# Optimization experiments

Measured on AMD Instinct MI355X. Metric: run time of the kernel, lower is better.

Reference implementation:

```python
import jax, jax.numpy as jnp
import numpy as np

EPS = 1e-12
LAMDA = 1.0
MAX_ITER = 10


def setup_inputs() -> dict:
    key = jax.random.key(0)
    k1, k2 = jax.random.split(key)
    B, L1, L2, D = 64, 1024, 1024, 256
    x1 = jax.random.normal(k1, (B, L1, D), dtype=jnp.float32)
    x2 = jax.random.normal(k2, (B, L2, D), dtype=jnp.float32)
    return {"x1": x1, "x2": x2}


def _cos(x1, x2):
    # batched cosine similarity: [B, L1, L2]
    M = jnp.einsum('bik,bjk->bij', x1, x2)
    a = jnp.sqrt(jnp.sum(x1 * x1, axis=-1, keepdims=True))  # [B, L1, 1]
    b = jnp.sqrt(jnp.sum(x2 * x2, axis=-1, keepdims=True))  # [B, L2, 1]
    norm = a * jnp.swapaxes(b, 1, 2)                          # [B, L1, L2]
    return M / (norm + EPS)


def reference(x1, x2):
    B, L1, _ = x1.shape
    L2 = x2.shape[1]
    M = 1.0 - _cos(x1, x2)          # [B, L1, L2] cost matrix
    K = jnp.exp(-M * LAMDA)
    w1 = jnp.full((B, L1, 1), 1.0 / L1, dtype=x1.dtype)
    w2 = jnp.full((B, L2, 1), 1.0 / L2, dtype=x1.dtype)
    ui = jnp.ones((B, L1, 1), dtype=x1.dtype)
    vi = jnp.ones((B, L2, 1), dtype=x1.dtype)
    Kt = jnp.swapaxes(K, 1, 2)      # [B, L2, L1]

    def body(_, carry):
        ui, vi = carry
        vi = w2 / (jnp.matmul(Kt, ui) + EPS)
        ui = w1 / (jnp.matmul(K, vi) + EPS)
        return (ui, vi)

    ui, vi = jax.lax.fori_loop(0, MAX_ITER, body, (ui, vi))
    G = ui * K * jnp.swapaxes(vi, 1, 2)   # transport plan [B, L1, L2]
    G_max = jnp.max(G, axis=(-1, -2), keepdims=True)
    G_min = jnp.min(G, axis=(-1, -2), keepdims=True)
    G = (G - G_min) / (G_max - G_min + EPS)
    return G * M
```

## Files before the change

kernel.cpp:

```cpp
#include <hip/hip_runtime.h>
#include <hip/hip_bf16.h>
#include <hip/hip_fp8.h>


#define EPSV 1e-12f
#define W1 0.0009765625f

typedef short  short8 __attribute__((ext_vector_type(8)));
typedef float  f32x4  __attribute__((ext_vector_type(4)));
typedef float  f32x2v __attribute__((ext_vector_type(2)));

__device__ __forceinline__ float rcpf_(float x) {
#if __has_builtin(__builtin_amdgcn_rcpf)
  return __builtin_amdgcn_rcpf(x);
#else
  return 1.0f / x;
#endif
}
__device__ __forceinline__ float rsqf_(float x) {
#if __has_builtin(__builtin_amdgcn_rsqf)
  return __builtin_amdgcn_rsqf(x);
#else
  return rsqrtf(x);
#endif
}

__device__ __forceinline__ unsigned char enc1(float x) {
#if __has_builtin(__builtin_amdgcn_cvt_pk_fp8_f32)
  int v = __builtin_amdgcn_cvt_pk_fp8_f32(x, x, 0, false);
  return (unsigned char)(v & 0xff);
#else
  __hip_fp8_e4m3 q(x); return (unsigned char)q.__x;
#endif
}
__device__ __forceinline__ float dec1(unsigned char b) {
#if __has_builtin(__builtin_amdgcn_cvt_f32_fp8)
  return __builtin_amdgcn_cvt_f32_fp8((int)b, 0);
#else
  __hip_fp8_e4m3 q; q.__x = (__hip_fp8_storage_t)b; return (float)q;
#endif
}
__device__ __forceinline__ unsigned pack4fp8(float a, float b, float c, float d) {
#if __has_builtin(__builtin_amdgcn_cvt_pk_fp8_f32)
  int v = __builtin_amdgcn_cvt_pk_fp8_f32(a, b, 0, false);
  v = __builtin_amdgcn_cvt_pk_fp8_f32(c, d, v, true);
  return (unsigned)v;
#else
  return (unsigned)enc1(a) | ((unsigned)enc1(b) << 8) |
         ((unsigned)enc1(c) << 16) | ((unsigned)enc1(d) << 24);
#endif
}
__device__ __forceinline__ void unpack4fp8(unsigned v, float* f) {
#if __has_builtin(__builtin_amdgcn_cvt_pk_f32_fp8)
  f32x2v p;
  p = __builtin_amdgcn_cvt_pk_f32_fp8((int)v, false); f[0] = p[0]; f[1] = p[1];
  p = __builtin_amdgcn_cvt_pk_f32_fp8((int)v, true);  f[2] = p[0]; f[3] = p[1];
#else
  #pragma unroll
  for (int i = 0; i < 4; ++i) f[i] = dec1((unsigned char)((v >> (i * 8)) & 0xff));
#endif
}
__device__ __forceinline__ void decode16(uint4 d, float* f) {
  unpack4fp8(d.x, f); unpack4fp8(d.y, f + 4);
  unpack4fp8(d.z, f + 8); unpack4fp8(d.w, f + 12);
}
__device__ __forceinline__ float dot16u(uint4 d, const float* s) {
#if __has_builtin(__builtin_amdgcn_cvt_pk_f32_fp8)
  f32x2v p; float a = 0.f;
  p = __builtin_amdgcn_cvt_pk_f32_fp8((int)d.x, false); a += p[0]*s[0]  + p[1]*s[1];
  p = __builtin_amdgcn_cvt_pk_f32_fp8((int)d.x, true);  a += p[0]*s[2]  + p[1]*s[3];
  p = __builtin_amdgcn_cvt_pk_f32_fp8((int)d.y, false); a += p[0]*s[4]  + p[1]*s[5];
  p = __builtin_amdgcn_cvt_pk_f32_fp8((int)d.y, true);  a += p[0]*s[6]  + p[1]*s[7];
  p = __builtin_amdgcn_cvt_pk_f32_fp8((int)d.z, false); a += p[0]*s[8]  + p[1]*s[9];
  p = __builtin_amdgcn_cvt_pk_f32_fp8((int)d.z, true);  a += p[0]*s[10] + p[1]*s[11];
  p = __builtin_amdgcn_cvt_pk_f32_fp8((int)d.w, false); a += p[0]*s[12] + p[1]*s[13];
  p = __builtin_amdgcn_cvt_pk_f32_fp8((int)d.w, true);  a += p[0]*s[14] + p[1]*s[15];
  return a;
#else
  float f[16]; decode16(d, f);
  float a = 0.f;
  #pragma unroll
  for (int k = 0; k < 16; ++k) a += f[k] * s[k];
  return a;
#endif
}
__device__ __forceinline__ void axpy16u(uint4 d, float u, float* pacc) {
#if __has_builtin(__builtin_amdgcn_cvt_pk_f32_fp8)
  f32x2v p;
  p = __builtin_amdgcn_cvt_pk_f32_fp8((int)d.x, false); pacc[0]  += p[0]*u; pacc[1]  += p[1]*u;
  p = __builtin_amdgcn_cvt_pk_f32_fp8((int)d.x, true);  pacc[2]  += p[0]*u; pacc[3]  += p[1]*u;
  p = __builtin_amdgcn_cvt_pk_f32_fp8((int)d.y, false); pacc[4]  += p[0]*u; pacc[5]  += p[1]*u;
  p = __builtin_amdgcn_cvt_pk_f32_fp8((int)d.y, true);  pacc[6]  += p[0]*u; pacc[7]  += p[1]*u;
  p = __builtin_amdgcn_cvt_pk_f32_fp8((int)d.z, false); pacc[8]  += p[0]*u; pacc[9]  += p[1]*u;
  p = __builtin_amdgcn_cvt_pk_f32_fp8((int)d.z, true);  pacc[10] += p[0]*u; pacc[11] += p[1]*u;
  p = __builtin_amdgcn_cvt_pk_f32_fp8((int)d.w, false); pacc[12] += p[0]*u; pacc[13] += p[1]*u;
  p = __builtin_amdgcn_cvt_pk_f32_fp8((int)d.w, true);  pacc[14] += p[0]*u; pacc[15] += p[1]*u;
#else
  float f[16]; decode16(d, f);
  #pragma unroll
  for (int k = 0; k < 16; ++k) pacc[k] += f[k] * u;
#endif
}

__device__ __forceinline__ short8 ld_cvt8_sq(const float* p, float* sq) {
  float4 f0 = *(const float4*)p;
  float4 f1 = *(const float4*)(p + 4);
  *sq += f0.x * f0.x + f0.y * f0.y + f0.z * f0.z + f0.w * f0.w
       + f1.x * f1.x + f1.y * f1.y + f1.z * f1.z + f1.w * f1.w;
  float2 p0; p0.x = f0.x; p0.y = f0.y;
  float2 p1; p1.x = f0.z; p1.y = f0.w;
  float2 p2; p2.x = f1.x; p2.y = f1.y;
  float2 p3; p3.x = f1.z; p3.y = f1.w;
  __hip_bfloat162 h0 = __float22bfloat162_rn(p0);
  __hip_bfloat162 h1 = __float22bfloat162_rn(p1);
  __hip_bfloat162 h2_ = __float22bfloat162_rn(p2);
  __hip_bfloat162 h3 = __float22bfloat162_rn(p3);
  short2 a = *(short2*)&h0, b = *(short2*)&h1, c = *(short2*)&h2_, d = *(short2*)&h3;
  short8 r;
  r[0] = a.x; r[1] = a.y; r[2] = b.x; r[3] = b.y;
  r[4] = c.x; r[5] = c.y; r[6] = d.x; r[7] = d.y;
  return r;
}

__global__ __launch_bounds__(256) void diag_kernel(float* __restrict__ out,
                                                   float val, int n) {
  int stride = gridDim.x * 256;
  for (int i = blockIdx.x * 256 + threadIdx.x; i < n; i += stride) out[i] = val;
}

__global__ __launch_bounds__(256) void gemm_kernel(
    const float* __restrict__ x1, const float* __restrict__ x2,
    unsigned char* __restrict__ K8g, unsigned char* __restrict__ R8g,
    unsigned* __restrict__ mm, _Float16* __restrict__ p0) {
  __shared__ __align__(16) unsigned short smem[2 * 128 * 64];
  __shared__ float asq[128], bsq[128];
  __shared__ float csum[4][128];
  unsigned short* As = smem;
  unsigned short* Bs = smem + 128 * 64;
  int bid = blockIdx.x;
  int b = bid >> 6, tile = bid & 63;
  int ti = (tile >> 3) << 7, tj = (tile & 7) << 7;
  int t = threadIdx.x, lane = t & 63, wave = t >> 6;
  int wr = (wave >> 1) << 6, wc = (wave & 1) << 6;
  const float* Ag = x1 + ((size_t)(b * 1024 + ti)) * 256;
  const float* Bg = x2 + ((size_t)(b * 1024 + tj)) * 256;

  if (bid == 0 && t < 128) mm[t] = (t < 64) ? 0u : 0x7f800000u;

  f32x4 acc[4][4];
  f32x4 zero = {0.f, 0.f, 0.f, 0.f};
  #pragma unroll
  for (int m = 0; m < 4; ++m)
    #pragma unroll
    for (int n = 0; n < 4; ++n) acc[m][n] = zero;

  float sqa[4] = {0.f, 0.f, 0.f, 0.f};
  float sqb[4] = {0.f, 0.f, 0.f, 0.f};
  short8 ra[4], rb[4];
  #pragma unroll
  for (int c = 0; c < 4; ++c) {
    int ch = t + (c << 8); int row = ch >> 3, kg = ch & 7;
    ra[c] = ld_cvt8_sq(Ag + row * 256 + kg * 8, &sqa[c]);
    rb[c] = ld_cvt8_sq(Bg + row * 256 + kg * 8, &sqb[c]);
  }

  for (int k0 = 0; k0 < 4; ++k0) {
    __syncthreads();
    #pragma unroll
    for (int c = 0; c < 4; ++c) {
      int ch = t + (c << 8); int row = ch >> 3, kg = ch & 7;
      int kgs = kg ^ (row & 7);
      *(short8*)(As + row * 64 + kgs * 8) = ra[c];
      *(short8*)(Bs + row * 64 + kgs * 8) = rb[c];
    }
    __syncthreads();
    if (k0 < 3) {
      #pragma unroll
      for (int c = 0; c < 4; ++c) {
        int ch = t + (c << 8); int row = ch >> 3, kg = ch & 7;
        ra[c] = ld_cvt8_sq(Ag + row * 256 + (k0 + 1) * 64 + kg * 8, &sqa[c]);
        rb[c] = ld_cvt8_sq(Bg + row * 256 + (k0 + 1) * 64 + kg * 8, &sqb[c]);
      }
    }
    #pragma unroll
    for (int ks = 0; ks < 2; ++ks) {
      short8 af[4], bfr[4];
      #pragma unroll
      for (int m = 0; m < 4; ++m) {
        int row = wr + m * 16 + (lane & 15);
        int c16 = (ks << 2) + (lane >> 4);
        af[m] = *(const short8*)(As + row * 64 + ((c16 ^ (row & 7)) << 3));
      }
      #pragma unroll
      for (int n = 0; n < 4; ++n) {
        int row = wc + n * 16 + (lane & 15);
        int c16 = (ks << 2) + (lane >> 4);
        bfr[n] = *(const short8*)(Bs + row * 64 + ((c16 ^ (row & 7)) << 3));
      }
      #pragma unroll
      for (int m = 0; m < 4; ++m)
        #pragma unroll
        for (int n = 0; n < 4; ++n)
          acc[m][n] = __builtin_amdgcn_mfma_f32_16x16x32_bf16(bfr[n], af[m], acc[m][n], 0, 0, 0);
    }
  }
  __syncthreads();
  #pragma unroll
  for (int c = 0; c < 4; ++c) {
    float sa = sqa[c], sb = sqb[c];
    sa += __shfl_xor(sa, 1, 64); sb += __shfl_xor(sb, 1, 64);
    sa += __shfl_xor(sa, 2, 64); sb += __shfl_xor(sb, 2, 64);
    sa += __shfl_xor(sa, 4, 64); sb += __shfl_xor(sb, 4, 64);
    if ((t & 7) == 0) {
      int row = (t + (c << 8)) >> 3;
      asq[row] = sa; bsq[row] = sb;
    }
  }
  __syncthreads();

  float ira[4];
  #pragma unroll
  for (int m = 0; m < 4; ++m)
    ira[m] = rsqf_(asq[wr + m * 16 + (lane & 15)]);
  float irb[4][4];
  #pragma unroll
  for (int n = 0; n < 4; ++n)
    #pragma unroll
    for (int q = 0; q < 4; ++q)
      irb[n][q] = rsqf_(bsq[wc + n * 16 + ((lane >> 4) << 2) + q]);
  float csn[4][4];
  #pragma unroll
  for (int n = 0; n < 4; ++n)
    #pragma unroll
    for (int q = 0; q < 4; ++q) csn[n][q] = 0.f;
  size_t kbase = ((size_t)b << 20);
  #pragma unroll
  for (int m = 0; m < 4; ++m) {
    size_t rowoff = kbase + (size_t)(ti + wr + m * 16 + (lane & 15)) * 1024 + tj + wc + ((lane >> 4) << 2);
    #pragma unroll
    for (int n = 0; n < 4; ++n) {
      float kv[4];
      #pragma unroll
      for (int q = 0; q < 4; ++q) {
        float cosv = acc[m][n][q] * ira[m] * irb[n][q];
        kv[q] = __expf(cosv - 1.0f);
        csn[n][q] += kv[q];
      }
      unsigned pk = pack4fp8(kv[0], kv[1], kv[2], kv[3]);
      float kd[4];
      unpack4fp8(pk, kd);
      float rr[4];
      #pragma unroll
      for (int q = 0; q < 4; ++q) rr[q] = kv[q] * rcpf_(kd[q]) - 1.0f;
      unsigned pr = pack4fp8(rr[0], rr[1], rr[2], rr[3]);
      *(unsigned*)(K8g + rowoff + n * 16) = pk;
      *(unsigned*)(R8g + rowoff + n * 16) = pr;
    }
  }
  #pragma unroll
  for (int n = 0; n < 4; ++n)
    #pragma unroll
    for (int q = 0; q < 4; ++q) {
      float c_ = csn[n][q];
      c_ += __shfl_xor(c_, 1, 64);
      c_ += __shfl_xor(c_, 2, 64);
      c_ += __shfl_xor(c_, 4, 64);
      c_ += __shfl_xor(c_, 8, 64);
      if ((lane & 15) == 0)
        csum[wave][wc + n * 16 + ((lane >> 4) << 2) + q] = c_;
    }
  __syncthreads();
  if (t < 128) {
    float s_ = csum[t >> 6][t] + csum[2 + (t >> 6)][t];
    p0[((size_t)b << 13) + ((size_t)(ti >> 7) << 10) + tj + t] = (_Float16)s_;
  }
}

template<int BSHIFT, int NSRC>
__global__ __launch_bounds__(1024) void fused1024_kernel(
    const unsigned char* __restrict__ K8, const _Float16* __restrict__ src,
    _Float16* __restrict__ dst) {
  int bid = blockIdx.x;
  int b = bid >> 2, s = bid & 3;
  int t = threadIdx.x, lane = t & 63, w = t >> 6;
  __shared__ float sv[1024];
  __shared__ float plds[8][1024];
  {
    int col = t;
    const _Float16* sp = src + ((size_t)b << BSHIFT) + col;
    float y = 0.f;
    #pragma unroll
    for (int j = 0; j < NSRC; ++j) y += (float)sp[j << 10];
    sv[col] = W1 / (y + EPSV);
  }
  __syncthreads();
  float svr[16];
  {
    float4 s0 = *(const float4*)&sv[lane * 16];
    float4 s1 = *(const float4*)&sv[lane * 16 + 4];
    float4 s2 = *(const float4*)&sv[lane * 16 + 8];
    float4 s3 = *(const float4*)&sv[lane * 16 + 12];
    svr[0] = s0.x;  svr[1] = s0.y;  svr[2]  = s0.z;  svr[3]  = s0.w;
    svr[4] = s1.x;  svr[5] = s1.y;  svr[6]  = s1.z;  svr[7]  = s1.w;
    svr[8] = s2.x;  svr[9] = s2.y;  svr[10] = s2.z;  svr[11] = s2.w;
    svr[12] = s3.x; svr[13] = s3.y; svr[14] = s3.z;  svr[15] = s3.w;
  }
  float pacc[16];
  #pragma unroll
  for (int k = 0; k < 16; ++k) pacc[k] = 0.f;
  const unsigned char* kp = K8 + ((size_t)b << 20) + (size_t)(s * 256 + w) * 1024 + lane * 16;
  uint4 c0 = *(const uint4*)(kp);
  uint4 c1 = *(const uint4*)(kp + 16384);
  for (int p = 0; p < 8; ++p) {
    uint4 n0, n1_;
    if (p < 7) {
      n0 = *(const uint4*)(kp + (size_t)(2 * p + 2) * 16384);
      n1_ = *(const uint4*)(kp + (size_t)(2 * p + 3) * 16384);
    }
    float d0 = dot16u(c0, svr);
    float d1 = dot16u(c1, svr);
    #pragma unroll
    for (int off = 1; off < 64; off <<= 1) {
      d0 += __shfl_xor(d0, off, 64);
      d1 += __shfl_xor(d1, off, 64);
    }
    float u0 = W1 / (d0 + EPSV);
    float u1 = W1 / (d1 + EPSV);
    axpy16u(c0, u0, pacc);
    axpy16u(c1, u1, pacc);
    c0 = n0; c1 = n1_;
  }
  if (w < 8) {
    *(float4*)&plds[w][lane * 16]      = *(float4*)&pacc[0];
    *(float4*)&plds[w][lane * 16 + 4]  = *(float4*)&pacc[4];
    *(float4*)&plds[w][lane * 16 + 8]  = *(float4*)&pacc[8];
    *(float4*)&plds[w][lane * 16 + 12] = *(float4*)&pacc[12];
  }
  __syncthreads();
  if (w >= 8) {
    float* pl = &plds[w - 8][lane * 16];
    #pragma unroll
    for (int k = 0; k < 16; ++k) pl[k] += pacc[k];
  }
  __syncthreads();
  {
    int col = t;
    float sum = 0.f;
    #pragma unroll
    for (int i = 0; i < 8; ++i) sum += plds[i][col];
    dst[((size_t)b << 12) + (s << 10) + col] = (_Float16)sum;
  }
}

template<int FINAL>
__global__ __launch_bounds__(512) void fused512_kernel(
    const unsigned char* __restrict__ K8, const unsigned char* __restrict__ R8,
    const _Float16* __restrict__ src, _Float16* __restrict__ dst,
    float* __restrict__ zb, unsigned* __restrict__ mm) {
  int bid = blockIdx.x;
  int b = bid >> 2, s = bid & 3;
  int t = threadIdx.x, lane = t & 63, w = t >> 6;
  __shared__ float sv[1024];
  __shared__ float plds[8][1024];
  __shared__ float red[16];
  #pragma unroll
  for (int p = 0; p < 2; ++p) {
    int col = (p << 9) + t;
    const _Float16* sp = src + ((size_t)b << 12) + col;
    float y = (float)sp[0] + (float)sp[1024] + (float)sp[2048] + (float)sp[3072];
    sv[col] = W1 / (y + EPSV);
  }
  __syncthreads();
  float svr[16];
  {
    float4 s0 = *(const float4*)&sv[lane * 16];
    float4 s1 = *(const float4*)&sv[lane * 16 + 4];
    float4 s2 = *(const float4*)&sv[lane * 16 + 8];
    float4 s3 = *(const float4*)&sv[lane * 16 + 12];
    svr[0] = s0.x;  svr[1] = s0.y;  svr[2]  = s0.z;  svr[3]  = s0.w;
    svr[4] = s1.x;  svr[5] = s1.y;  svr[6]  = s1.z;  svr[7]  = s1.w;
    svr[8] = s2.x;  svr[9] = s2.y;  svr[10] = s2.z;  svr[11] = s2.w;
    svr[12] = s3.x; svr[13] = s3.y; svr[14] = s3.z;  svr[15] = s3.w;
  }
  float pacc[16];
  #pragma unroll
  for (int k = 0; k < 16; ++k) pacc[k] = 0.f;
  float gmn = 3.4e38f, gmx = 0.f;
  const unsigned char* kp = K8 + ((size_t)b << 20) + (size_t)(s * 256 + w) * 1024 + lane * 16;
  const unsigned char* rp = R8 + ((size_t)b << 20) + (size_t)(s * 256 + w) * 1024 + lane * 16;
  uint4 c0 = *(const uint4*)(kp);
  uint4 c1 = *(const uint4*)(kp + 8192);
  uint4 r0 = *(const uint4*)(rp);
  uint4 r1 = *(const uint4*)(rp + 8192);
  for (int p = 0; p < 16; ++p) {
    uint4 n0, n1_, q0, q1;
    if (p < 15) {
      n0 = *(const uint4*)(kp + (size_t)(2 * p + 2) * 8192);
      n1_ = *(const uint4*)(kp + (size_t)(2 * p + 3) * 8192);
      q0 = *(const uint4*)(rp + (size_t)(2 * p + 2) * 8192);
      q1 = *(const uint4*)(rp + (size_t)(2 * p + 3) * 8192);
    }
    float kf0[16], kf1[16];
    decode16(c0, kf0);
    decode16(c1, kf1);
    {
      float rf0[16], rf1[16];
      decode16(r0, rf0);
      decode16(r1, rf1);
      #pragma unroll
      for (int k = 0; k < 16; ++k) {
        kf0[k] *= (1.0f + rf0[k]);
        kf1[k] *= (1.0f + rf1[k]);
      }
    }
    float d0 = 0.f, d1 = 0.f;
    #pragma unroll
    for (int k = 0; k < 16; ++k) {
      d0 += kf0[k] * svr[k];
      d1 += kf1[k] * svr[k];
    }
    #pragma unroll
    for (int off = 1; off < 64; off <<= 1) {
      d0 += __shfl_xor(d0, off, 64);
      d1 += __shfl_xor(d1, off, 64);
    }
    float u0 = W1 / (d0 + EPSV);
    float u1 = W1 / (d1 + EPSV);
    if (FINAL) {
      if (lane == 0) {
        zb[(b << 10) + s * 256 + w + (2 * p) * 8] = d0;
        zb[(b << 10) + s * 256 + w + (2 * p + 1) * 8] = d1;
      }
      #pragma unroll
      for (int k = 0; k < 16; ++k) {
        float g0 = u0 * kf0[k] * svr[k];
        float g1 = u1 * kf1[k] * svr[k];
        gmn = fminf(gmn, fminf(g0, g1));
        gmx = fmaxf(gmx, fmaxf(g0, g1));
      }
    } else {
      #pragma unroll
      for (int k = 0; k < 16; ++k)
        pacc[k] += kf0[k] * u0 + kf1[k] * u1;
    }
    c0 = n0; c1 = n1_; r0 = q0; r1 = q1;
  }
  if (!FINAL) {
    *(float4*)&plds[w][lane * 16]      = *(float4*)&pacc[0];
    *(float4*)&plds[w][lane * 16 + 4]  = *(float4*)&pacc[4];
    *(float4*)&plds[w][lane * 16 + 8]  = *(float4*)&pacc[8];
    *(float4*)&plds[w][lane * 16 + 12] = *(float4*)&pacc[12];
    __syncthreads();
    #pragma unroll
    for (int p = 0; p < 2; ++p) {
      int col = (p << 9) + t;
      float sum = plds[0][col] + plds[1][col] + plds[2][col] + plds[3][col]
                + plds[4][col] + plds[5][col] + plds[6][col] + plds[7][col];
      dst[((size_t)b << 12) + (s << 10) + col] = (_Float16)sum;
    }
  } else {
    #pragma unroll
    for (int off = 1; off < 64; off <<= 1) {
      gmn = fminf(gmn, __shfl_xor(gmn, off, 64));
      gmx = fmaxf(gmx, __shfl_xor(gmx, off, 64));
    }
    if (lane == 0) { red[w] = gmn; red[8 + w] = gmx; }
    __syncthreads();
    if (t == 0) {
      float m0 = red[0], m1 = red[8];
      #pragma unroll
      for (int i = 1; i < 8; ++i) { m0 = fminf(m0, red[i]); m1 = fmaxf(m1, red[8 + i]); }
      atomicMin(&mm[64 + b], __float_as_uint(m0));
      atomicMax(&mm[b],      __float_as_uint(m1));
    }
  }
}

__global__ __launch_bounds__(256) void fin_kernel(
    const unsigned char* __restrict__ K8, const unsigned char* __restrict__ R8,
    const _Float16* __restrict__ src, const float* __restrict__ zb,
    const unsigned* __restrict__ mm, float* __restrict__ out) {
  int bid = blockIdx.x;
  int b = bid >> 4, rg = bid & 15;
  int t = threadIdx.x, lane = t & 63, w = t >> 6;
  __shared__ float sv[1024];
  #pragma unroll
  for (int p = 0; p < 4; ++p) {
    int col = (p << 8) + t;
    const _Float16* sp = src + ((size_t)b << 12) + col;
    float y = (float)sp[0] + (float)sp[1024] + (float)sp[2048] + (float)sp[3072];
    sv[col] = W1 / (y + EPSV);
  }
  __syncthreads();
  float svr[16];
  {
    float4 s0 = *(const float4*)&sv[lane * 16];
    float4 s1 = *(const float4*)&sv[lane * 16 + 4];
    float4 s2 = *(const float4*)&sv[lane * 16 + 8];
    float4 s3 = *(const float4*)&sv[lane * 16 + 12];
    svr[0] = s0.x;  svr[1] = s0.y;  svr[2]  = s0.z;  svr[3]  = s0.w;
    svr[4] = s1.x;  svr[5] = s1.y;  svr[6]  = s1.z;  svr[7]  = s1.w;
    svr[8] = s2.x;  svr[9] = s2.y;  svr[10] = s2.z;  svr[11] = s2.w;
    svr[12] = s3.x; svr[13] = s3.y; svr[14] = s3.z;  svr[15] = s3.w;
  }
  float gmx = __uint_as_float(mm[b]);
  float gmn = __uint_as_float(mm[64 + b]);
  float scale = 1.0f / (gmx - gmn + EPSV);
  const unsigned char* kp = K8 + ((size_t)b << 20) + (size_t)(rg * 64 + w) * 1024 + lane * 16;
  const unsigned char* rp = R8 + ((size_t)b << 20) + (size_t)(rg * 64 + w) * 1024 + lane * 16;
  float* op = out + ((size_t)b << 20) + (size_t)(rg * 64 + w) * 1024 + lane * 16;
  for (int it = 0; it < 16; ++it) {
    int r = rg * 64 + w + it * 4;
    float u = W1 / (zb[b * 1024 + r] + EPSV);
    uint4 dk = *(const uint4*)(kp + (size_t)it * 4096);
    uint4 dr = *(const uint4*)(rp + (size_t)it * 4096);
    float kf[16], rf[16], o[16];
    decode16(dk, kf);
    decode16(dr, rf);
    #pragma unroll
    for (int k = 0; k < 16; ++k) {
      float krec = kf[k] * (1.0f + rf[k]);
      float g = u * krec * svr[k];
      o[k] = (g - gmn) * scale * (-__logf(krec));
    }
    *(float4*)(op + (size_t)it * 4096)      = *(float4*)&o[0];
    *(float4*)(op + (size_t)it * 4096 + 4)  = *(float4*)&o[4];
    *(float4*)(op + (size_t)it * 4096 + 8)  = *(float4*)&o[8];
    *(float4*)(op + (size_t)it * 4096 + 12) = *(float4*)&o[12];
  }
}

extern "C" void kernel_launch(void* const* d_in, const int* in_sizes, int n_in,
                              void* d_out, int out_size, void* d_ws, size_t ws_size,
                              hipStream_t stream) {
  const float* x1 = (const float*)d_in[0];
  const float* x2 = (const float*)d_in[1];
  float* out = (float*)d_out;
  char* ws = (char*)d_ws;

  unsigned char* K8g = (unsigned char*)ws;
  unsigned char* R8g = (unsigned char*)(ws + 67108864ULL);
  float*    zb = (float*)(ws + 134217728ULL);
  _Float16* p0 = (_Float16*)(ws + 134217728ULL);
  _Float16* pA = (_Float16*)(ws + 134742016ULL);
  _Float16* pB = (_Float16*)(ws + 135266304ULL);
  unsigned* mm = (unsigned*)(ws + 135790592ULL);
  const size_t WS_NEED = 135791104ULL;

  if (ws_size < WS_NEED) {
    float val = 100.0f + (float)(ws_size >> 20);
    diag_kernel<<<2048, 256, 0, stream>>>(out, val, out_size);
    return;
  }

  gemm_kernel<<<4096, 256, 0, stream>>>(x1, x2, K8g, R8g, mm, p0);
  fused1024_kernel<13, 8><<<256, 1024, 0, stream>>>(K8g, p0, pB);
  for (int k = 2; k <= 8; ++k) {
    _Float16* src = (k & 1) ? pA : pB;
    _Float16* dst = (k & 1) ? pB : pA;
    fused1024_kernel<12, 4><<<256, 1024, 0, stream>>>(K8g, src, dst);
  }
  fused512_kernel<0><<<256, 512, 0, stream>>>(K8g, R8g, pA, pB, zb, mm);
  fused512_kernel<1><<<256, 512, 0, stream>>>(K8g, R8g, pB, pA, zb, mm);
  fin_kernel<<<1024, 256, 0, stream>>>(K8g, R8g, pB, zb, mm, out);
}
```

Before: 448.3 us.

## Stage fp32 GEMM tiles via direct global-to-LDS loads and drop fused512 pass

The GEMM kernel now copies fp32 tiles of x1/x2 straight into swizzled LDS using global_load_lds, then converts them to bf16 and accumulates the squared norms while reading LDS. This replaces the register-staged prefetch-and-convert path. The K-step shrinks to 32 with no double buffering, so each step ends in a barrier. The host also runs one extra fused1024 iteration in place of the first fused512_kernel launch, which changes the Sinkhorn schedule and needs the buffer ping-pong to still line up.

```diff
diff --git a/kernel.cpp b/kernel.cpp
--- a/kernel.cpp
+++ b/kernel.cpp
@@ -22,6 +22,16 @@
   return __builtin_amdgcn_rsqf(x);
 #else
   return rsqrtf(x);
+#endif
+}
+
+__device__ __forceinline__ void dma16(const float* g, float* l, int laneByte) {
+#if __has_builtin(__builtin_amdgcn_global_load_lds)
+  __builtin_amdgcn_global_load_lds(
+      (const __attribute__((address_space(1))) unsigned*)g,
+      (__attribute__((address_space(3))) unsigned*)l, 16, 0, 0);
+#else
+  *(float4*)((char*)l + laneByte) = *(const float4*)g;
 #endif
 }
 
@@ -102,11 +112,7 @@
 #endif
 }
 
-__device__ __forceinline__ short8 ld_cvt8_sq(const float* p, float* sq) {
-  float4 f0 = *(const float4*)p;
-  float4 f1 = *(const float4*)(p + 4);
-  *sq += f0.x * f0.x + f0.y * f0.y + f0.z * f0.z + f0.w * f0.w
-       + f1.x * f1.x + f1.y * f1.y + f1.z * f1.z + f1.w * f1.w;
+__device__ __forceinline__ short8 cvt8f(float4 f0, float4 f1) {
   float2 p0; p0.x = f0.x; p0.y = f0.y;
   float2 p1; p1.x = f0.z; p1.y = f0.w;
   float2 p2; p2.x = f1.x; p2.y = f1.y;
@@ -132,11 +138,10 @@
     const float* __restrict__ x1, const float* __restrict__ x2,
     unsigned char* __restrict__ K8g, unsigned char* __restrict__ R8g,
     unsigned* __restrict__ mm, _Float16* __restrict__ p0) {
-  __shared__ __align__(16) unsigned short smem[2 * 128 * 64];
-  __shared__ float asq[128], bsq[128];
+  __shared__ __align__(16) float As[128 * 32];
+  __shared__ __align__(16) float Bs[128 * 32];
+  __shared__ float bsq[128];
   __shared__ float csum[4][128];
-  unsigned short* As = smem;
-  unsigned short* Bs = smem + 128 * 64;
   int bid = blockIdx.x;
   int b = bid >> 6, tile = bid & 63;
   int ti = (tile >> 3) << 7, tj = (tile & 7) << 7;
@@ -156,72 +161,67 @@
 
   float sqa[4] = {0.f, 0.f, 0.f, 0.f};
   float sqb[4] = {0.f, 0.f, 0.f, 0.f};
-  short8 ra[4], rb[4];
-  #pragma unroll
-  for (int c = 0; c < 4; ++c) {
-    int ch = t + (c << 8); int row = ch >> 3, kg = ch & 7;
-    ra[c] = ld_cvt8_sq(Ag + row * 256 + kg * 8, &sqa[c]);
-    rb[c] = ld_cvt8_sq(Bg + row * 256 + kg * 8, &sqb[c]);
-  }
-
-  for (int k0 = 0; k0 < 4; ++k0) {
+
+  int srow = (wave << 5) + (lane >> 3);
+  int pg = (lane & 7) ^ ((srow & 3) << 1);
+  const float* gA = Ag + (size_t)srow * 256 + pg * 4;
+  const float* gB = Bg + (size_t)srow * 256 + pg * 4;
+  int laneByte = lane * 16;
+  float* lA = &As[(wave << 5) * 32];
+  float* lB = &Bs[(wave << 5) * 32];
+
+  for (int k0 = 0; k0 < 8; ++k0) {
+    #pragma unroll
+    for (int j = 0; j < 4; ++j) {
+      dma16(gA + j * 2048 + k0 * 32, lA + j * 8 * 32, laneByte);
+      dma16(gB + j * 2048 + k0 * 32, lB + j * 8 * 32, laneByte);
+    }
     __syncthreads();
-    #pragma unroll
-    for (int c = 0; c < 4; ++c) {
-      int ch = t + (c << 8); int row = ch >> 3, kg = ch & 7;
-      int kgs = kg ^ (row & 7);
-      *(short8*)(As + row * 64 + kgs * 8) = ra[c];
-      *(short8*)(Bs + row * 64 + kgs * 8) = rb[c];
-    }
+    short8 af[4], bfr[4];
+    #pragma unroll
+    for (int m = 0; m < 4; ++m) {
+      int r = wr + m * 16 + (lane & 15);
+      int c = (lane >> 4) ^ (r & 3);
+      float4 a0 = *(const float4*)&As[r * 32 + c * 8];
+      float4 a1 = *(const float4*)&As[r * 32 + c * 8 + 4];
+      sqa[m] += a0.x*a0.x + a0.y*a0.y + a0.z*a0.z + a0.w*a0.w
+              + a1.x*a1.x + a1.y*a1.y + a1.z*a1.z + a1.w*a1.w;
+      af[m] = cvt8f(a0, a1);
+    }
+    #pragma unroll
+    for (int n = 0; n < 4; ++n) {
+      int r = wc + n * 16 + (lane & 15);
+      int c = (lane >> 4) ^ (r & 3);
+      float4 b0 = *(const float4*)&Bs[r * 32 + c * 8];
+      float4 b1 = *(const float4*)&Bs[r * 32 + c * 8 + 4];
+      sqb[n] += b0.x*b0.x + b0.y*b0.y + b0.z*b0.z + b0.w*b0.w
+              + b1.x*b1.x + b1.y*b1.y + b1.z*b1.z + b1.w*b1.w;
+      bfr[n] = cvt8f(b0, b1);
+    }
+    #pragma unroll
+    for (int m = 0; m < 4; ++m)
+      #pragma unroll
+      for (int n = 0; n < 4; ++n)
+        acc[m][n] = __builtin_amdgcn_mfma_f32_16x16x32_bf16(bfr[n], af[m], acc[m][n], 0, 0, 0);
     __syncthreads();
-    if (k0 < 3) {
-      #pragma unroll
-      for (int c = 0; c < 4; ++c) {
-        int ch = t + (c << 8); int row = ch >> 3, kg = ch & 7;
-        ra[c] = ld_cvt8_sq(Ag + row * 256 + (k0 + 1) * 64 + kg * 8, &sqa[c]);
-        rb[c] = ld_cvt8_sq(Bg + row * 256 + (k0 + 1) * 64 + kg * 8, &sqb[c]);
-      }
-    }
-    #pragma unroll
-    for (int ks = 0; ks < 2; ++ks) {
-      short8 af[4], bfr[4];
-      #pragma unroll
-      for (int m = 0; m < 4; ++m) {
-        int row = wr + m * 16 + (lane & 15);
-        int c16 = (ks << 2) + (lane >> 4);
-        af[m] = *(const short8*)(As + row * 64 + ((c16 ^ (row & 7)) << 3));
-      }
-      #pragma unroll
-      for (int n = 0; n < 4; ++n) {
-        int row = wc + n * 16 + (lane & 15);
-        int c16 = (ks << 2) + (lane >> 4);
-        bfr[n] = *(const short8*)(Bs + row * 64 + ((c16 ^ (row & 7)) << 3));
-      }
-      #pragma unroll
-      for (int m = 0; m < 4; ++m)
-        #pragma unroll
-        for (int n = 0; n < 4; ++n)
-          acc[m][n] = __builtin_amdgcn_mfma_f32_16x16x32_bf16(bfr[n], af[m], acc[m][n], 0, 0, 0);
-    }
-  }
-  __syncthreads();
-  #pragma unroll
-  for (int c = 0; c < 4; ++c) {
-    float sa = sqa[c], sb = sqb[c];
-    sa += __shfl_xor(sa, 1, 64); sb += __shfl_xor(sb, 1, 64);
-    sa += __shfl_xor(sa, 2, 64); sb += __shfl_xor(sb, 2, 64);
-    sa += __shfl_xor(sa, 4, 64); sb += __shfl_xor(sb, 4, 64);
-    if ((t & 7) == 0) {
-      int row = (t + (c << 8)) >> 3;
-      asq[row] = sa; bsq[row] = sb;
-    }
+  }
+
+  #pragma unroll
+  for (int m = 0; m < 4; ++m) {
+    sqa[m] += __shfl_xor(sqa[m], 16, 64);
+    sqa[m] += __shfl_xor(sqa[m], 32, 64);
+    sqb[m] += __shfl_xor(sqb[m], 16, 64);
+    sqb[m] += __shfl_xor(sqb[m], 32, 64);
+  }
+  if ((lane >> 4) == 0) {
+    #pragma unroll
+    for (int n = 0; n < 4; ++n) bsq[wc + n * 16 + (lane & 15)] = sqb[n];
   }
   __syncthreads();
 
   float ira[4];
   #pragma unroll
-  for (int m = 0; m < 4; ++m)
-    ira[m] = rsqf_(asq[wr + m * 16 + (lane & 15)]);
+  for (int m = 0; m < 4; ++m) ira[m] = rsqf_(sqa[m]);
   float irb[4][4];
   #pragma unroll
   for (int n = 0; n < 4; ++n)
@@ -555,12 +555,11 @@
 
   gemm_kernel<<<4096, 256, 0, stream>>>(x1, x2, K8g, R8g, mm, p0);
   fused1024_kernel<13, 8><<<256, 1024, 0, stream>>>(K8g, p0, pB);
-  for (int k = 2; k <= 8; ++k) {
+  for (int k = 2; k <= 9; ++k) {
     _Float16* src = (k & 1) ? pA : pB;
     _Float16* dst = (k & 1) ? pB : pA;
     fused1024_kernel<12, 4><<<256, 1024, 0, stream>>>(K8g, src, dst);
   }
-  fused512_kernel<0><<<256, 512, 0, stream>>>(K8g, R8g, pA, pB, zb, mm);
   fused512_kernel<1><<<256, 512, 0, stream>>>(K8g, R8g, pB, pA, zb, mm);
   fin_kernel<<<1024, 256, 0, stream>>>(K8g, R8g, pB, zb, mm, out);
 }
```

New measurement: 464.2 us. +3.5%, slower.

## Drop residual-corrected non-final Sinkhorn pass and run final pass with 1024 threads

Applied to the files above, without the earlier changes.

The ninth Sinkhorn half-iteration now uses the cheaper fused1024 kernel that reads only the 8-bit K, instead of the 512-thread kernel that also reads the residual R8 correction. The final pass, which still applies the residual, is rewritten as a 1024-thread kernel with 16 waves and no software-prefetched register double buffering. This cuts memory traffic for one full pass over R8 and raises occupancy, at the risk of some accuracy loss from one more low-precision iteration and less load latency hiding.

```diff
diff --git a/kernel.cpp b/kernel.cpp
--- a/kernel.cpp
+++ b/kernel.cpp
@@ -352,20 +352,17 @@
   }
 }
 
-template<int FINAL>
-__global__ __launch_bounds__(512) void fused512_kernel(
+__global__ __launch_bounds__(1024) void fused1024F_kernel(
     const unsigned char* __restrict__ K8, const unsigned char* __restrict__ R8,
-    const _Float16* __restrict__ src, _Float16* __restrict__ dst,
-    float* __restrict__ zb, unsigned* __restrict__ mm) {
+    const _Float16* __restrict__ src, float* __restrict__ zb,
+    unsigned* __restrict__ mm) {
   int bid = blockIdx.x;
   int b = bid >> 2, s = bid & 3;
   int t = threadIdx.x, lane = t & 63, w = t >> 6;
   __shared__ float sv[1024];
-  __shared__ float plds[8][1024];
-  __shared__ float red[16];
-  #pragma unroll
-  for (int p = 0; p < 2; ++p) {
-    int col = (p << 9) + t;
+  __shared__ float red[32];
+  {
+    int col = t;
     const _Float16* sp = src + ((size_t)b << 12) + col;
     float y = (float)sp[0] + (float)sp[1024] + (float)sp[2048] + (float)sp[3072];
     sv[col] = W1 / (y + EPSV);
@@ -382,37 +379,23 @@
     svr[8] = s2.x;  svr[9] = s2.y;  svr[10] = s2.z;  svr[11] = s2.w;
     svr[12] = s3.x; svr[13] = s3.y; svr[14] = s3.z;  svr[15] = s3.w;
   }
-  float pacc[16];
-  #pragma unroll
-  for (int k = 0; k < 16; ++k) pacc[k] = 0.f;
   float gmn = 3.4e38f, gmx = 0.f;
   const unsigned char* kp = K8 + ((size_t)b << 20) + (size_t)(s * 256 + w) * 1024 + lane * 16;
   const unsigned char* rp = R8 + ((size_t)b << 20) + (size_t)(s * 256 + w) * 1024 + lane * 16;
-  uint4 c0 = *(const uint4*)(kp);
-  uint4 c1 = *(const uint4*)(kp + 8192);
-  uint4 r0 = *(const uint4*)(rp);
-  uint4 r1 = *(const uint4*)(rp + 8192);
-  for (int p = 0; p < 16; ++p) {
-    uint4 n0, n1_, q0, q1;
-    if (p < 15) {
-      n0 = *(const uint4*)(kp + (size_t)(2 * p + 2) * 8192);
-      n1_ = *(const uint4*)(kp + (size_t)(2 * p + 3) * 8192);
-      q0 = *(const uint4*)(rp + (size_t)(2 * p + 2) * 8192);
-      q1 = *(const uint4*)(rp + (size_t)(2 * p + 3) * 8192);
-    }
-    float kf0[16], kf1[16];
+  for (int p = 0; p < 8; ++p) {
+    uint4 c0 = *(const uint4*)(kp + (size_t)(2 * p) * 16384);
+    uint4 c1 = *(const uint4*)(kp + (size_t)(2 * p + 1) * 16384);
+    uint4 r0 = *(const uint4*)(rp + (size_t)(2 * p) * 16384);
+    uint4 r1 = *(const uint4*)(rp + (size_t)(2 * p + 1) * 16384);
+    float kf0[16], kf1[16], rf[16];
     decode16(c0, kf0);
+    decode16(r0, rf);
+    #pragma unroll
+    for (int k = 0; k < 16; ++k) kf0[k] *= (1.0f + rf[k]);
     decode16(c1, kf1);
-    {
-      float rf0[16], rf1[16];
-      decode16(r0, rf0);
-      decode16(r1, rf1);
-      #pragma unroll
-      for (int k = 0; k < 16; ++k) {
-        kf0[k] *= (1.0f + rf0[k]);
-        kf1[k] *= (1.0f + rf1[k]);
-      }
-    }
+    decode16(r1, rf);
+    #pragma unroll
+    for (int k = 0; k < 16; ++k) kf1[k] *= (1.0f + rf[k]);
     float d0 = 0.f, d1 = 0.f;
     #pragma unroll
     for (int k = 0; k < 16; ++k) {
@@ -426,53 +409,31 @@
     }
     float u0 = W1 / (d0 + EPSV);
     float u1 = W1 / (d1 + EPSV);
-    if (FINAL) {
-      if (lane == 0) {
-        zb[(b << 10) + s * 256 + w + (2 * p) * 8] = d0;
-        zb[(b << 10) + s * 256 + w + (2 * p + 1) * 8] = d1;
-      }
-      #pragma unroll
-      for (int k = 0; k < 16; ++k) {
-        float g0 = u0 * kf0[k] * svr[k];
-        float g1 = u1 * kf1[k] * svr[k];
-        gmn = fminf(gmn, fminf(g0, g1));
-        gmx = fmaxf(gmx, fmaxf(g0, g1));
-      }
-    } else {
-      #pragma unroll
-      for (int k = 0; k < 16; ++k)
-        pacc[k] += kf0[k] * u0 + kf1[k] * u1;
-    }
-    c0 = n0; c1 = n1_; r0 = q0; r1 = q1;
-  }
-  if (!FINAL) {
-    *(float4*)&plds[w][lane * 16]      = *(float4*)&pacc[0];
-    *(float4*)&plds[w][lane * 16 + 4]  = *(float4*)&pacc[4];
-    *(float4*)&plds[w][lane * 16 + 8]  = *(float4*)&pacc[8];
-    *(float4*)&plds[w][lane * 16 + 12] = *(float4*)&pacc[12];
-    __syncthreads();
-    #pragma unroll
-    for (int p = 0; p < 2; ++p) {
-      int col = (p << 9) + t;
-      float sum = plds[0][col] + plds[1][col] + plds[2][col] + plds[3][col]
-                + plds[4][col] + plds[5][col] + plds[6][col] + plds[7][col];
-      dst[((size_t)b << 12) + (s << 10) + col] = (_Float16)sum;
-    }
-  } else {
-    #pragma unroll
-    for (int off = 1; off < 64; off <<= 1) {
-      gmn = fminf(gmn, __shfl_xor(gmn, off, 64));
-      gmx = fmaxf(gmx, __shfl_xor(gmx, off, 64));
-    }
-    if (lane == 0) { red[w] = gmn; red[8 + w] = gmx; }
-    __syncthreads();
-    if (t == 0) {
-      float m0 = red[0], m1 = red[8];
-      #pragma unroll
-      for (int i = 1; i < 8; ++i) { m0 = fminf(m0, red[i]); m1 = fmaxf(m1, red[8 + i]); }
-      atomicMin(&mm[64 + b], __float_as_uint(m0));
-      atomicMax(&mm[b],      __float_as_uint(m1));
-    }
+    if (lane == 0) {
+      zb[(b << 10) + s * 256 + w + (2 * p) * 16] = d0;
+      zb[(b << 10) + s * 256 + w + (2 * p + 1) * 16] = d1;
+    }
+    #pragma unroll
+    for (int k = 0; k < 16; ++k) {
+      float g0 = u0 * kf0[k] * svr[k];
+      float g1 = u1 * kf1[k] * svr[k];
+      gmn = fminf(gmn, fminf(g0, g1));
+      gmx = fmaxf(gmx, fmaxf(g0, g1));
+    }
+  }
+  #pragma unroll
+  for (int off = 1; off < 64; off <<= 1) {
+    gmn = fminf(gmn, __shfl_xor(gmn, off, 64));
+    gmx = fmaxf(gmx, __shfl_xor(gmx, off, 64));
+  }
+  if (lane == 0) { red[w] = gmn; red[16 + w] = gmx; }
+  __syncthreads();
+  if (t == 0) {
+    float m0 = red[0], m1 = red[16];
+    #pragma unroll
+    for (int i = 1; i < 16; ++i) { m0 = fminf(m0, red[i]); m1 = fmaxf(m1, red[16 + i]); }
+    atomicMin(&mm[64 + b], __float_as_uint(m0));
+    atomicMax(&mm[b],      __float_as_uint(m1));
   }
 }
 
@@ -555,12 +516,11 @@
 
   gemm_kernel<<<4096, 256, 0, stream>>>(x1, x2, K8g, R8g, mm, p0);
   fused1024_kernel<13, 8><<<256, 1024, 0, stream>>>(K8g, p0, pB);
-  for (int k = 2; k <= 8; ++k) {
+  for (int k = 2; k <= 9; ++k) {
     _Float16* src = (k & 1) ? pA : pB;
     _Float16* dst = (k & 1) ? pB : pA;
     fused1024_kernel<12, 4><<<256, 1024, 0, stream>>>(K8g, src, dst);
   }
-  fused512_kernel<0><<<256, 512, 0, stream>>>(K8g, R8g, pA, pB, zb, mm);
-  fused512_kernel<1><<<256, 512, 0, stream>>>(K8g, R8g, pB, pA, zb, mm);
+  fused1024F_kernel<<<256, 1024, 0, stream>>>(K8g, R8g, pB, zb, mm);
   fin_kernel<<<1024, 256, 0, stream>>>(K8g, R8g, pB, zb, mm, out);
 }
```

After: 434.6 us (median of 2 runs). 3.1% less time.
